# Performance work log

Measured on AMD Instinct MI355X. Metric: run time of the kernel, lower is better.

The kernel has to match this reference:

```python
import jax, jax.numpy as jnp
import numpy as np

N = 100000   # active voxels (stride=1 -> output coords == input coords)
C_IN = 64
C_OUT = 64
K3 = 27      # 3x3x3 kernel offsets
M = 40000    # rulebook pairs per kernel offset
EPS = 1e-5


def setup_inputs() -> dict:
    key = jax.random.key(0)
    k1, k2, k3, k4 = jax.random.split(key, 4)
    x = jax.random.normal(k1, (N, C_IN), dtype=jnp.float32)
    # conv weights per kernel offset: [K3, inc, outc]
    W = jax.random.normal(k2, (K3, C_IN, C_OUT), dtype=jnp.float32) * 0.05
    gamma = jnp.ones((C_OUT,), dtype=jnp.float32)
    beta = jnp.zeros((C_OUT,), dtype=jnp.float32)
    # rulebook: for each offset k, M (input_idx, output_idx) pairs
    in_idx = jax.random.randint(k3, (K3, M), 0, N, dtype=jnp.int32)
    out_idx = jax.random.randint(k4, (K3, M), 0, N, dtype=jnp.int32)
    return {"x": x, "W": W, "gamma": gamma, "beta": beta,
            "in_idx": in_idx, "out_idx": out_idx}


def reference(x, W, gamma, beta, in_idx, out_idx):
    n_out = x.shape[0]  # stride=1: output voxel set == input voxel set
    # gather: [K3, M, C_IN]
    feat = x[in_idx]
    # batched GEMM over kernel offsets: [K3, M, C_OUT]
    contrib = jnp.einsum('kmi,kio->kmo', feat, W)
    # scatter-add into output voxels
    out = jnp.zeros((n_out, W.shape[2]), dtype=x.dtype)
    out = out.at[out_idx.reshape(-1)].add(contrib.reshape(-1, W.shape[2]))
    # BatchNorm over active points (training-mode batch stats, biased var)
    mean = jnp.mean(out, axis=0)
    var = jnp.mean(jnp.square(out - mean), axis=0)
    y = (out - mean) * jax.lax.rsqrt(var + EPS) * gamma + beta
    # ReLU
    return jnp.maximum(y, 0.0)
```

## Files before the change

### kernel.cpp

```cpp
#include <hip/hip_runtime.h>


#define N_VOX   100000
#define NPAD    100096
#define K3      27
#define M_PAIRS 40000
#define NPAIRS  (K3 * M_PAIRS)
#define BN_EPS  1e-5f
#define NBINS   (K3 * NPAD)
#define AUXMAX  184320
#define AUXCAP  (AUXMAX - 1)
#define ZROW    (N_VOX + AUXMAX - 1)
#define SENT    0xFFFFFFFFFFFFFFFFull
#define MFLAG   (1ull << 63)

#define OFF_WT     0u
#define OFF_STATS  221184u
#define OFF_CTRS   221696u
#define OFF_GINX   221760u
#define OFF_NODE   11032128u
#define OFF_LIST   19672128u
#define OFF_XB     21146688u
#define OFF_BH     (OFF_XB + 12800000u)
#define WS_NEED    ((size_t)OFF_XB + (size_t)(N_VOX + AUXMAX) * 128u)

#define NB_WT    432
#define NB_XB    3125
#define NB_BUILD 4219
#define GRID_IB  (NB_WT + NB_XB + 1 + NB_BUILD)

typedef __attribute__((ext_vector_type(8))) short bf16x8;
typedef __attribute__((ext_vector_type(4))) float f32x4;
typedef unsigned long long u64;

__device__ __forceinline__ short f2bf(float f) {
  unsigned u = __builtin_bit_cast(unsigned, f);
  u += 0x7FFFu + ((u >> 16) & 1u);
  return (short)(u >> 16);
}
__device__ __forceinline__ float bf2f(short s) {
  unsigned u = ((unsigned)(unsigned short)s) << 16;
  return __builtin_bit_cast(float, u);
}

__global__ __launch_bounds__(256) void init_build_kernel(const float* __restrict__ W,
                                                         const float* __restrict__ x,
                                                         const int* __restrict__ in_idx,
                                                         const int* __restrict__ out_idx,
                                                         short* __restrict__ wt,
                                                         short* __restrict__ xb,
                                                         u64* __restrict__ bh,
                                                         u64* __restrict__ node) {
  int b = blockIdx.x, t = threadIdx.x;
  if (b < NB_WT) {
    int id = b * 256 + t;
    int k = id >> 12, rem = id & 4095, c = rem >> 6, i = rem & 63;
    wt[id] = f2bf(W[(k << 12) + (i << 6) + c]);
  } else if (b < NB_WT + NB_XB) {
    int id = (b - NB_WT) * 256 + t;
    if (id < N_VOX * 8) {
      float4 lo = ((const float4*)x)[id * 2];
      float4 hi = ((const float4*)x)[id * 2 + 1];
      bf16x8 v;
      v[0] = f2bf(lo.x); v[1] = f2bf(lo.y); v[2] = f2bf(lo.z); v[3] = f2bf(lo.w);
      v[4] = f2bf(hi.x); v[5] = f2bf(hi.y); v[6] = f2bf(hi.z); v[7] = f2bf(hi.w);
      ((bf16x8*)xb)[id] = v;
    }
  } else if (b == NB_WT + NB_XB) {
    if (t < 8) {
      bf16x8 z = {0, 0, 0, 0, 0, 0, 0, 0};
      ((bf16x8*)(xb + (size_t)ZROW * 64))[t] = z;
    }
  } else {
    int id = (b - (NB_WT + NB_XB + 1)) * 256 + t;
    if (id < NPAIRS) {
      int k  = id / M_PAIRS;
      int in = in_idx[id];
      int o  = out_idx[id];
      int bb = k * NPAD + o;
      u64 nh  = ((u64)(unsigned)in << 32) | (unsigned)id;
      u64 old = atomicExch(&bh[bb], nh);
      node[id] = old;
      if (old != SENT) atomicOr(&bh[bb], MFLAG);
    }
  }
}

__global__ __launch_bounds__(256) void compact_kernel(const u64* __restrict__ bh,
                                                      int* __restrict__ ginx,
                                                      u64* __restrict__ list,
                                                      int* __restrict__ ctrs) {
  __shared__ int l_cnt, l_base;
  int t = threadIdx.x;
  if (t == 0) l_cnt = 0;
  __syncthreads();
  int w = blockIdx.x * 256 + t;
  bool ok = (w < NBINS / 4);
  u64 h[4];
  if (ok) {
    ulonglong2 p0 = ((const ulonglong2*)bh)[w * 2];
    ulonglong2 p1 = ((const ulonglong2*)bh)[w * 2 + 1];
    h[0] = p0.x; h[1] = p0.y; h[2] = p1.x; h[3] = p1.y;
  } else {
    h[0] = SENT; h[1] = SENT; h[2] = SENT; h[3] = SENT;
  }
  int gv[4], lp[4];
  #pragma unroll
  for (int s = 0; s < 4; ++s) {
    lp[s] = -1;
    if (h[s] == SENT)            gv[s] = ZROW;
    else if (!(h[s] >> 63))      gv[s] = (int)((h[s] >> 32) & 0x7FFFFFFFu);
    else                         lp[s] = atomicAdd(&l_cnt, 1);
  }
  __syncthreads();
  if (t == 0) l_base = (l_cnt > 0) ? atomicAdd(&ctrs[0], l_cnt) : 0;
  __syncthreads();
  #pragma unroll
  for (int s = 0; s < 4; ++s) {
    if (lp[s] >= 0) {
      int pos = l_base + lp[s];
      if (pos < AUXCAP) { list[pos] = h[s]; gv[s] = N_VOX + pos; }
      else              { gv[s] = (int)((h[s] >> 32) & 0x7FFFFFFFu); }
    }
  }
  if (ok) ((int4*)ginx)[w] = make_int4(gv[0], gv[1], gv[2], gv[3]);
}

__global__ __launch_bounds__(256) void fixup_kernel(short* __restrict__ xb,
                                                    const u64* __restrict__ list,
                                                    const u64* __restrict__ node,
                                                    const int* __restrict__ ctrs) {
  int n = ctrs[0]; if (n > AUXCAP) n = AUXCAP;
  int wid  = (blockIdx.x * 256 + threadIdx.x) >> 6;
  int lane = threadIdx.x & 63;
  int nw   = gridDim.x * 4;
  for (int i = wid; i < n; i += nw) {
    u64 h = list[i];
    int in0     = (int)((h >> 32) & 0x7FFFFFFFu);
    unsigned id = (unsigned)(h & 0xFFFFFFFFu);
    float acc = bf2f(xb[(size_t)in0 * 64 + lane]);
    u64 v = node[id];
    while (v != SENT) {
      int in = (int)((v >> 32) & 0x7FFFFFFFu);
      id = (unsigned)(v & 0xFFFFFFFFu);
      acc += bf2f(xb[(size_t)in * 64 + lane]);
      v = node[id];
    }
    xb[(size_t)(N_VOX + i) * 64 + lane] = f2bf(acc);
  }
}

__global__ __launch_bounds__(256) void conv_out_kernel(const short* __restrict__ xb,
                                                       const short* __restrict__ wt,
                                                       const int* __restrict__ ginx,
                                                       float* __restrict__ out,
                                                       float* __restrict__ stats) {
  __shared__ short lds[2 * 4096];
  __shared__ float ls[128];
  int t = threadIdx.x, wave = t >> 6, lane = t & 63;
  int g = lane >> 4, c0 = lane & 15, g8 = g * 8;
  int o0 = blockIdx.x * 128 + wave * 32 + c0;
  int o1 = o0 + 16;

  int rb  = ((c0 * 128 + g * 16) ^ ((c0 & 7) << 4)) >> 1;
  int wb0 = ((t * 32) ^ (((t >> 2) & 7) << 4)) >> 1;
  if (t < 128) ls[t] = 0.f;

  f32x4 acc0[4], acc1[4];
  #pragma unroll
  for (int n = 0; n < 4; ++n) {
    acc0[n][0]=0.f; acc0[n][1]=0.f; acc0[n][2]=0.f; acc0[n][3]=0.f;
    acc1[n][0]=0.f; acc1[n][1]=0.f; acc1[n][2]=0.f; acc1[n][3]=0.f;
  }

  bf16x8 s0w = *(const bf16x8*)(wt + t * 16);
  bf16x8 s1w = *(const bf16x8*)(wt + t * 16 + 8);
  int ia = ginx[o0], ib = ginx[o1];
  const short* xa = xb + (size_t)ia * 64;
  const short* xc = xb + (size_t)ib * 64;
  bf16x8 a0c = *(const bf16x8*)(xa + g8);
  bf16x8 a1c = *(const bf16x8*)(xa + 32 + g8);
  bf16x8 a2c = *(const bf16x8*)(xc + g8);
  bf16x8 a3c = *(const bf16x8*)(xc + 32 + g8);
  int i1a = ginx[NPAD + o0], i1b = ginx[NPAD + o1];
  *(bf16x8*)&lds[wb0]     = s0w;
  *(bf16x8*)&lds[wb0 ^ 8] = s1w;
  __syncthreads();

  int buf = 0;
  for (int k = 0; k < K3; ++k) {
    if (k + 1 < K3) {
      const short* wn = wt + (size_t)(k + 1) * 4096 + t * 16;
      s0w = *(const bf16x8*)(wn);
      s1w = *(const bf16x8*)(wn + 8);
    }
    const short* pa = xb + (size_t)i1a * 64;
    const short* pb = xb + (size_t)i1b * 64;
    bf16x8 a0n = *(const bf16x8*)(pa + g8);
    bf16x8 a1n = *(const bf16x8*)(pa + 32 + g8);
    bf16x8 a2n = *(const bf16x8*)(pb + g8);
    bf16x8 a3n = *(const bf16x8*)(pb + 32 + g8);
    int i2a = ZROW, i2b = ZROW;
    if (k + 2 < K3) {
      i2a = ginx[(size_t)(k + 2) * NPAD + o0];
      i2b = ginx[(size_t)(k + 2) * NPAD + o1];
    }
    const short* lb = lds + buf * 4096;
    #pragma unroll
    for (int n = 0; n < 4; ++n) {
      bf16x8 b0 = *(const bf16x8*)&lb[rb + n * 1024];
      bf16x8 b1 = *(const bf16x8*)&lb[(rb ^ 32) + n * 1024];
      acc0[n] = __builtin_amdgcn_mfma_f32_16x16x32_bf16(a0c, b0, acc0[n], 0, 0, 0);
      acc0[n] = __builtin_amdgcn_mfma_f32_16x16x32_bf16(a1c, b1, acc0[n], 0, 0, 0);
      acc1[n] = __builtin_amdgcn_mfma_f32_16x16x32_bf16(a2c, b0, acc1[n], 0, 0, 0);
      acc1[n] = __builtin_amdgcn_mfma_f32_16x16x32_bf16(a3c, b1, acc1[n], 0, 0, 0);
    }
    if (k + 1 < K3) {
      short* wd = lds + (buf ^ 1) * 4096;
      *(bf16x8*)&wd[wb0]     = s0w;
      *(bf16x8*)&wd[wb0 ^ 8] = s1w;
    }
    __syncthreads();
    a0c = a0n; a1c = a1n; a2c = a2n; a3c = a3n;
    i1a = i2a; i1b = i2b; buf ^= 1;
  }

  int orow = blockIdx.x * 128 + wave * 32 + (g << 2);
  #pragma unroll
  for (int j = 0; j < 4; ++j) {
    int r0 = orow + j, r1 = orow + 16 + j;
    if (r0 < N_VOX) {
      float* op = out + (size_t)r0 * 64 + c0;
      op[0] = acc0[0][j]; op[16] = acc0[1][j]; op[32] = acc0[2][j]; op[48] = acc0[3][j];
    }
    if (r1 < N_VOX) {
      float* op = out + (size_t)r1 * 64 + c0;
      op[0] = acc1[0][j]; op[16] = acc1[1][j]; op[32] = acc1[2][j]; op[48] = acc1[3][j];
    }
  }

  #pragma unroll
  for (int n = 0; n < 4; ++n) {
    float s = 0.f, q = 0.f;
    #pragma unroll
    for (int j = 0; j < 4; ++j) {
      float v0 = acc0[n][j], v1 = acc1[n][j];
      s += v0 + v1; q += v0 * v0 + v1 * v1;
    }
    atomicAdd(&ls[n * 16 + c0], s);
    atomicAdd(&ls[64 + n * 16 + c0], q);
  }
  __syncthreads();
  if (t < 128) unsafeAtomicAdd(&stats[t], ls[t]);
}

__global__ __launch_bounds__(256) void norm_kernel(float* __restrict__ out,
                                                   const float* __restrict__ stats,
                                                   const float* __restrict__ gamma,
                                                   const float* __restrict__ beta) {
  int i4 = blockIdx.x * 256 + threadIdx.x;
  if (i4 >= N_VOX * 16) return;
  const float invN = 1.0f / (float)N_VOX;
  float4 v = ((const float4*)out)[i4];
  int c0 = (i4 << 2) & 63;
  float r[4] = {v.x, v.y, v.z, v.w};
  #pragma unroll
  for (int j = 0; j < 4; ++j) {
    int c = c0 + j;
    float mean = stats[c] * invN;
    float ex2  = stats[64 + c] * invN;
    float var  = ex2 - mean * mean;
    float scale = gamma[c] * rsqrtf(var + BN_EPS);
    float shift = beta[c] - mean * scale;
    r[j] = fmaxf(r[j] * scale + shift, 0.0f);
  }
  v.x = r[0]; v.y = r[1]; v.z = r[2]; v.w = r[3];
  ((float4*)out)[i4] = v;
}

extern "C" void kernel_launch(void* const* d_in, const int* in_sizes, int n_in,
                              void* d_out, int out_size, void* d_ws, size_t ws_size,
                              hipStream_t stream) {
  const float* x      = (const float*)d_in[0];
  const float* W      = (const float*)d_in[1];
  const float* gamma  = (const float*)d_in[2];
  const float* beta   = (const float*)d_in[3];
  const int*   in_idx = (const int*)d_in[4];
  const int*   out_idx= (const int*)d_in[5];
  float* out = (float*)d_out;

  char* ws = (char*)d_ws;
  short* wt    = (short*)(ws + OFF_WT);
  float* stats = (float*)(ws + OFF_STATS);
  int*   ctrs  = (int*)(ws + OFF_CTRS);
  int*   ginx  = (int*)(ws + OFF_GINX);
  u64*   node  = (u64*)(ws + OFF_NODE);
  u64*   list  = (u64*)(ws + OFF_LIST);
  short* xb    = (short*)(ws + OFF_XB);
  u64*   bh    = (u64*)(ws + OFF_BH);

  hipMemsetAsync(ws + OFF_STATS, 0, OFF_GINX - OFF_STATS, stream);
  hipMemsetAsync((void*)bh, 0xFF, (size_t)NBINS * 8, stream);

  init_build_kernel<<<GRID_IB, 256, 0, stream>>>(W, x, in_idx, out_idx,
                                                 wt, xb, bh, node);
  compact_kernel<<<(NBINS / 4 + 255) / 256, 256, 0, stream>>>(bh, ginx, list, ctrs);
  fixup_kernel<<<2048, 256, 0, stream>>>(xb, list, node, ctrs);
  conv_out_kernel<<<NPAD / 128, 256, 0, stream>>>(xb, wt, ginx, out, stats);
  norm_kernel<<<(N_VOX * 16 + 255) / 256, 256, 0, stream>>>(out, stats, gamma, beta);
}
```

Baseline: 235.9 us.

## Deepen gather prefetch to three stages and split init and build kernels

The conv kernel now keeps a three-deep ring of register buffers for gathered input rows. It fully unrolls the 27-offset loop so the rows are loaded two offsets ahead and their indices three ahead, which hides more gather latency behind the MFMAs. The fused init/build kernel is also split into two launches, one for the bf16 conversions and one for the atomic hash build. This costs more VGPRs, which may lower occupancy, and adds an extra kernel launch.

```diff
diff --git a/kernel.cpp b/kernel.cpp
--- a/kernel.cpp
+++ b/kernel.cpp
@@ -26,8 +26,8 @@
 
 #define NB_WT    432
 #define NB_XB    3125
+#define GRID_IN  (NB_WT + NB_XB + 1)
 #define NB_BUILD 4219
-#define GRID_IB  (NB_WT + NB_XB + 1 + NB_BUILD)
 
 typedef __attribute__((ext_vector_type(8))) short bf16x8;
 typedef __attribute__((ext_vector_type(4))) float f32x4;
@@ -43,14 +43,10 @@
   return __builtin_bit_cast(float, u);
 }
 
-__global__ __launch_bounds__(256) void init_build_kernel(const float* __restrict__ W,
-                                                         const float* __restrict__ x,
-                                                         const int* __restrict__ in_idx,
-                                                         const int* __restrict__ out_idx,
-                                                         short* __restrict__ wt,
-                                                         short* __restrict__ xb,
-                                                         u64* __restrict__ bh,
-                                                         u64* __restrict__ node) {
+__global__ __launch_bounds__(256) void init_kernel(const float* __restrict__ W,
+                                                   const float* __restrict__ x,
+                                                   short* __restrict__ wt,
+                                                   short* __restrict__ xb) {
   int b = blockIdx.x, t = threadIdx.x;
   if (b < NB_WT) {
     int id = b * 256 + t;
@@ -66,24 +62,28 @@
       v[4] = f2bf(hi.x); v[5] = f2bf(hi.y); v[6] = f2bf(hi.z); v[7] = f2bf(hi.w);
       ((bf16x8*)xb)[id] = v;
     }
-  } else if (b == NB_WT + NB_XB) {
+  } else {
     if (t < 8) {
       bf16x8 z = {0, 0, 0, 0, 0, 0, 0, 0};
       ((bf16x8*)(xb + (size_t)ZROW * 64))[t] = z;
     }
-  } else {
-    int id = (b - (NB_WT + NB_XB + 1)) * 256 + t;
-    if (id < NPAIRS) {
-      int k  = id / M_PAIRS;
-      int in = in_idx[id];
-      int o  = out_idx[id];
-      int bb = k * NPAD + o;
-      u64 nh  = ((u64)(unsigned)in << 32) | (unsigned)id;
-      u64 old = atomicExch(&bh[bb], nh);
-      node[id] = old;
-      if (old != SENT) atomicOr(&bh[bb], MFLAG);
-    }
-  }
+  }
+}
+
+__global__ __launch_bounds__(256) void build_kernel(const int* __restrict__ in_idx,
+                                                    const int* __restrict__ out_idx,
+                                                    u64* __restrict__ bh,
+                                                    u64* __restrict__ node) {
+  int id = blockIdx.x * 256 + threadIdx.x;
+  if (id >= NPAIRS) return;
+  int k  = id / M_PAIRS;
+  int in = in_idx[id];
+  int o  = out_idx[id];
+  int bb = k * NPAD + o;
+  u64 nh  = ((u64)(unsigned)in << 32) | (unsigned)id;
+  u64 old = atomicExch(&bh[bb], nh);
+  node[id] = old;
+  if (old != SENT) atomicOr(&bh[bb], MFLAG);
 }
 
 __global__ __launch_bounds__(256) void compact_kernel(const u64* __restrict__ bh,
@@ -150,6 +150,14 @@
   }
 }
 
+#define LOADST(S, ia, ib)                                       \
+  { const short* _pa = xb + (size_t)(ia) * 64;                  \
+    const short* _pb = xb + (size_t)(ib) * 64;                  \
+    S[0] = *(const bf16x8*)(_pa + g8);                          \
+    S[1] = *(const bf16x8*)(_pa + 32 + g8);                     \
+    S[2] = *(const bf16x8*)(_pb + g8);                          \
+    S[3] = *(const bf16x8*)(_pb + 32 + g8); }
+
 __global__ __launch_bounds__(256) void conv_out_kernel(const short* __restrict__ xb,
                                                        const short* __restrict__ wt,
                                                        const int* __restrict__ ginx,
@@ -173,47 +181,42 @@
     acc1[n][0]=0.f; acc1[n][1]=0.f; acc1[n][2]=0.f; acc1[n][3]=0.f;
   }
 
+  bf16x8 st[3][4];
   bf16x8 s0w = *(const bf16x8*)(wt + t * 16);
   bf16x8 s1w = *(const bf16x8*)(wt + t * 16 + 8);
-  int ia = ginx[o0], ib = ginx[o1];
-  const short* xa = xb + (size_t)ia * 64;
-  const short* xc = xb + (size_t)ib * 64;
-  bf16x8 a0c = *(const bf16x8*)(xa + g8);
-  bf16x8 a1c = *(const bf16x8*)(xa + 32 + g8);
-  bf16x8 a2c = *(const bf16x8*)(xc + g8);
-  bf16x8 a3c = *(const bf16x8*)(xc + 32 + g8);
-  int i1a = ginx[NPAD + o0], i1b = ginx[NPAD + o1];
+  {
+    int ia = ginx[o0], ib = ginx[o1];
+    LOADST(st[0], ia, ib);
+    ia = ginx[NPAD + o0]; ib = ginx[NPAD + o1];
+    LOADST(st[1], ia, ib);
+  }
+  int i2a = ginx[2 * NPAD + o0], i2b = ginx[2 * NPAD + o1];
   *(bf16x8*)&lds[wb0]     = s0w;
   *(bf16x8*)&lds[wb0 ^ 8] = s1w;
   __syncthreads();
 
   int buf = 0;
+  #pragma unroll
   for (int k = 0; k < K3; ++k) {
     if (k + 1 < K3) {
       const short* wn = wt + (size_t)(k + 1) * 4096 + t * 16;
       s0w = *(const bf16x8*)(wn);
       s1w = *(const bf16x8*)(wn + 8);
     }
-    const short* pa = xb + (size_t)i1a * 64;
-    const short* pb = xb + (size_t)i1b * 64;
-    bf16x8 a0n = *(const bf16x8*)(pa + g8);
-    bf16x8 a1n = *(const bf16x8*)(pa + 32 + g8);
-    bf16x8 a2n = *(const bf16x8*)(pb + g8);
-    bf16x8 a3n = *(const bf16x8*)(pb + 32 + g8);
-    int i2a = ZROW, i2b = ZROW;
-    if (k + 2 < K3) {
-      i2a = ginx[(size_t)(k + 2) * NPAD + o0];
-      i2b = ginx[(size_t)(k + 2) * NPAD + o1];
+    if (k + 2 < K3) LOADST(st[(k + 2) % 3], i2a, i2b);
+    if (k + 3 < K3) {
+      i2a = ginx[(size_t)(k + 3) * NPAD + o0];
+      i2b = ginx[(size_t)(k + 3) * NPAD + o1];
     }
     const short* lb = lds + buf * 4096;
     #pragma unroll
     for (int n = 0; n < 4; ++n) {
       bf16x8 b0 = *(const bf16x8*)&lb[rb + n * 1024];
       bf16x8 b1 = *(const bf16x8*)&lb[(rb ^ 32) + n * 1024];
-      acc0[n] = __builtin_amdgcn_mfma_f32_16x16x32_bf16(a0c, b0, acc0[n], 0, 0, 0);
-      acc0[n] = __builtin_amdgcn_mfma_f32_16x16x32_bf16(a1c, b1, acc0[n], 0, 0, 0);
-      acc1[n] = __builtin_amdgcn_mfma_f32_16x16x32_bf16(a2c, b0, acc1[n], 0, 0, 0);
-      acc1[n] = __builtin_amdgcn_mfma_f32_16x16x32_bf16(a3c, b1, acc1[n], 0, 0, 0);
+      acc0[n] = __builtin_amdgcn_mfma_f32_16x16x32_bf16(st[k % 3][0], b0, acc0[n], 0, 0, 0);
+      acc0[n] = __builtin_amdgcn_mfma_f32_16x16x32_bf16(st[k % 3][1], b1, acc0[n], 0, 0, 0);
+      acc1[n] = __builtin_amdgcn_mfma_f32_16x16x32_bf16(st[k % 3][2], b0, acc1[n], 0, 0, 0);
+      acc1[n] = __builtin_amdgcn_mfma_f32_16x16x32_bf16(st[k % 3][3], b1, acc1[n], 0, 0, 0);
     }
     if (k + 1 < K3) {
       short* wd = lds + (buf ^ 1) * 4096;
@@ -221,8 +224,7 @@
       *(bf16x8*)&wd[wb0 ^ 8] = s1w;
     }
     __syncthreads();
-    a0c = a0n; a1c = a1n; a2c = a2n; a3c = a3n;
-    i1a = i2a; i1b = i2b; buf ^= 1;
+    buf ^= 1;
   }
 
   int orow = blockIdx.x * 128 + wave * 32 + (g << 2);
@@ -302,8 +304,8 @@
   hipMemsetAsync(ws + OFF_STATS, 0, OFF_GINX - OFF_STATS, stream);
   hipMemsetAsync((void*)bh, 0xFF, (size_t)NBINS * 8, stream);
 
-  init_build_kernel<<<GRID_IB, 256, 0, stream>>>(W, x, in_idx, out_idx,
-                                                 wt, xb, bh, node);
+  init_kernel<<<GRID_IN, 256, 0, stream>>>(W, x, wt, xb);
+  build_kernel<<<NB_BUILD, 256, 0, stream>>>(in_idx, out_idx, bh, node);
   compact_kernel<<<(NBINS / 4 + 255) / 256, 256, 0, stream>>>(bh, ginx, list, ctrs);
   fixup_kernel<<<2048, 256, 0, stream>>>(xb, list, node, ctrs);
   conv_out_kernel<<<NPAD / 128, 256, 0, stream>>>(xb, wt, ginx, out, stats);
```

After: 218.1 us. 1.08x faster.
